# Optimization experiments

Measured on AMD Instinct MI355X. Metric: run time of the kernel, lower is better.

## Reference

```python
import jax, jax.numpy as jnp
import numpy as np

N, H, W = 128, 400, 400          # instances, feature canvas
MS = 28                          # mask_size = pooler_resolution*2
CT, CS = 80, 53                  # thing / stuff classes
STRIDE = 4                       # common_stride
HG, WG = 1600, 1600              # image-resolution gt panoptic
IGNORE = 255
LOSS_W = 1.0


def setup_inputs() -> dict:
    key = jax.random.key(0)
    ks = jax.random.split(key, 8)
    mask_logits = jax.random.normal(ks[0], (N, CT, MS, MS), jnp.float32)
    stuff_logit = jax.random.normal(ks[1], (CS, H, W), jnp.float32)
    thing_logit = jax.random.normal(ks[2], (CT, H, W), jnp.float32)
    # valid boxes in image pixel coords (x0,y0,x2,y2), width/height >= 16 px
    x0 = jax.random.uniform(ks[3], (N,), minval=0.0, maxval=1200.0)
    y0 = jax.random.uniform(ks[4], (N,), minval=0.0, maxval=1200.0)
    wh = jax.random.uniform(ks[5], (N, 2), minval=16.0, maxval=400.0)
    x2 = jnp.minimum(x0 + wh[:, 0], WG - 1.0)
    y2 = jnp.minimum(y0 + wh[:, 1], HG - 1.0)
    bbox = jnp.stack([x0, y0, x2, y2], axis=1).astype(jnp.float32)
    cls_idx = jax.random.randint(ks[6], (N,), 0, CT, dtype=jnp.int32)
    gt_panoptic = jax.random.randint(ks[7], (HG, WG), 0, CS + N, dtype=jnp.int32)
    return {"mask_logits": mask_logits, "stuff_logit": stuff_logit,
            "thing_logit": thing_logit, "bbox": bbox, "cls_idx": cls_idx,
            "gt_panoptic": gt_panoptic}


def _axis_sample(lo, size, grid, src_size):
    """Bilinear sampling coords along one axis (align_corners=False).
    lo: [N] box start (feat px, int); size: [N] box extent; grid: [G].
    Returns (idx0, idx1, frac) each [N, G]."""
    dst = grid[None, :].astype(jnp.float32) - lo[:, None].astype(jnp.float32)
    src = (dst + 0.5) * (src_size / size[:, None].astype(jnp.float32)) - 0.5
    f = jnp.floor(src)
    t = src - f
    i0 = jnp.clip(f, 0, src_size - 1).astype(jnp.int32)
    i1 = jnp.clip(f + 1, 0, src_size - 1).astype(jnp.int32)
    return i0, i1, t


def reference(mask_logits, stuff_logit, thing_logit, bbox, cls_idx, gt_panoptic):
    # _separate_fetch_logits: gather per-instance class channel -> [N, MS, MS]
    ml = mask_logits[jnp.arange(N), cls_idx]

    # _unmap_mask_logit_single: boxes -> feat coords (.long() == floor, boxes >= 0)
    bl = jnp.floor(bbox / STRIDE).astype(jnp.int32)
    x0b, y0b, x2b, y2b = bl[:, 0], bl[:, 1], bl[:, 2], bl[:, 3]
    hh = y2b - y0b + 1
    ww = x2b - x0b + 1
    ys = jnp.arange(H, dtype=jnp.int32)
    xs = jnp.arange(W, dtype=jnp.int32)

    i0, i1, ty = _axis_sample(y0b, hh, ys, MS)   # [N, H]
    j0, j1, tx = _axis_sample(x0b, ww, xs, MS)   # [N, W]

    # separable bilinear: rows [N, H, MS] then cols [N, H, W]
    r0 = jnp.take_along_axis(ml, jnp.broadcast_to(i0[:, :, None], (N, H, MS)), axis=1)
    r1 = jnp.take_along_axis(ml, jnp.broadcast_to(i1[:, :, None], (N, H, MS)), axis=1)
    rows = r0 * (1.0 - ty)[:, :, None] + r1 * ty[:, :, None]
    c0 = jnp.take_along_axis(rows, jnp.broadcast_to(j0[:, None, :], (N, H, W)), axis=2)
    c1 = jnp.take_along_axis(rows, jnp.broadcast_to(j1[:, None, :], (N, H, W)), axis=2)
    val = c0 * (1.0 - tx)[:, None, :] + c1 * tx[:, None, :]

    vy = (ys[None, :] >= jnp.maximum(y0b, 0)[:, None]) & (ys[None, :] <= jnp.minimum(y2b, H - 1)[:, None])
    vx = (xs[None, :] >= jnp.maximum(x0b, 0)[:, None]) & (xs[None, :] <= jnp.minimum(x2b, W - 1)[:, None])
    thing_mask_logit = jnp.where(vy[:, :, None] & vx[:, None, :], val, 0.0)

    # _crop_thing_logit_single: int()/round() based crop window
    bf = bbox / STRIDE
    cx1 = bf[:, 0].astype(jnp.int32)
    cy1 = bf[:, 1].astype(jnp.int32)
    cx2 = (jnp.round(bf[:, 2]) + 1.0).astype(jnp.int32)
    cy2 = (jnp.round(bf[:, 3]) + 1.0).astype(jnp.int32)
    my = (ys[None, :] >= cy1[:, None]) & (ys[None, :] < cy2[:, None])
    mx = (xs[None, :] >= cx1[:, None]) & (xs[None, :] < cx2[:, None])
    thing_sem_logit = jnp.where(my[:, :, None] & mx[:, None, :], thing_logit[cls_idx], 0.0)

    pan_logit = jnp.concatenate(
        [stuff_logit[None], (thing_mask_logit + thing_sem_logit)[None]], axis=1)

    # gt nearest-downsample to feat_size, then CE with ignore_index
    iy = jnp.floor(jnp.arange(H) * (HG / H)).astype(jnp.int32)
    ix = jnp.floor(jnp.arange(W) * (WG / W)).astype(jnp.int32)
    gt_ds = gt_panoptic[iy[:, None], ix[None, :]][None]          # [1, H, W]
    logp = jax.nn.log_softmax(pan_logit, axis=1)
    tgt = jnp.clip(gt_ds, 0, CS + N - 1)
    nll = -jnp.take_along_axis(logp, tgt[:, None], axis=1)[:, 0]  # [1, H, W]
    valid = gt_ds != IGNORE
    pan_loss = LOSS_W * jnp.sum(jnp.where(valid, nll, 0.0)) / jnp.maximum(
        jnp.sum(valid).astype(jnp.float32), 1.0)
    return pan_logit, pan_loss
```

## Files before the change

kernel.cpp:

```cpp
#include <hip/hip_runtime.h>
#include <hip/hip_bf16.h>
#include <math.h>

#define N_   128
#define H_   400
#define W_   400
#define MS_  28
#define CT_  80
#define CS_  53
#define HW_  (H_*W_)
#define NCH_ (CS_ + N_)
#define WG_  1600
#define IGN_ 255
#define G_   8
#define CPG_ 23

struct NParam {
  int vy_lo, vy_hi, vx_lo, vx_hi;
  int cy1, cy2, cx1, cx2;
  float sy, sx;
  int y0b, x0b;
  int mlbase, thbase;
  int pad0, pad1;
};

__device__ NParam g_par[N_];
__device__ float  g_acc[2];
__device__ float  g_pm[G_*HW_];
__device__ float  g_ps[G_*HW_];

__global__ void prep_kernel(const float* __restrict__ bbox,
                            const int*   __restrict__ cls_idx) {
  int n = threadIdx.x;
  if (n < 2) g_acc[n] = 0.0f;
  if (n >= N_) return;
  float b0 = bbox[4*n+0]*0.25f, b1 = bbox[4*n+1]*0.25f,
        b2 = bbox[4*n+2]*0.25f, b3 = bbox[4*n+3]*0.25f;
  int x0b = (int)floorf(b0), y0b = (int)floorf(b1);
  int x2b = (int)floorf(b2), y2b = (int)floorf(b3);
  int hh = y2b - y0b + 1, ww = x2b - x0b + 1;
  NParam p;
  p.vy_lo = max(y0b, 0); p.vy_hi = min(y2b, H_-1);
  p.vx_lo = max(x0b, 0); p.vx_hi = min(x2b, W_-1);
  p.cy1 = (int)b1; p.cx1 = (int)b0;
  p.cy2 = (int)(rintf(b3) + 1.0f);
  p.cx2 = (int)(rintf(b2) + 1.0f);
  p.sy = 28.0f / (float)hh; p.sx = 28.0f / (float)ww;
  p.y0b = y0b; p.x0b = x0b;
  int cls = cls_idx[n];
  p.mlbase = (n*CT_ + cls)*(MS_*MS_);
  p.thbase = cls*HW_;
  p.pad0 = 0; p.pad1 = 0;
  g_par[n] = p;
}

__device__ __forceinline__ void lse_update(float v, float& m, float& s) {
  float d = v - m;
  float e = __expf(-fabsf(d));
  s = (d > 0.0f) ? fmaf(s, e, 1.0f) : (s + e);
  m = fmaxf(m, v);
}

__global__ __launch_bounds__(256) void main_kernel(
    const float* __restrict__ mask_logits,
    const float* __restrict__ stuff_logit,
    const float* __restrict__ thing_logit,
    float* __restrict__ out)
{
  int pix = blockIdx.x*256 + threadIdx.x;
  int y = pix / W_;
  int x = pix - y*W_;
  int grp = blockIdx.y;
  int c0 = grp*CPG_;
  int c1 = min(NCH_, c0 + CPG_);

  float m = -INFINITY, s = 0.0f;

  int c = c0;
  for (; c < min(c1, CS_); ++c) {
    float v = stuff_logit[c*HW_ + pix];
    out[c*HW_ + pix] = v;
    lse_update(v, m, s);
  }
  for (; c < c1; ++c) {
    int n = c - CS_;
    NParam p = g_par[n];
    float v = 0.0f;
    if (y >= p.cy1 && y < p.cy2 && x >= p.cx1 && x < p.cx2)
      v = thing_logit[p.thbase + pix];
    if (y >= p.vy_lo && y <= p.vy_hi && x >= p.vx_lo && x <= p.vx_hi) {
      float srcy = ((float)(y - p.y0b) + 0.5f)*p.sy - 0.5f;
      float fy = floorf(srcy); float ty = srcy - fy;
      int i0 = (int)fminf(fmaxf(fy,        0.0f), (float)(MS_-1));
      int i1 = (int)fminf(fmaxf(fy + 1.0f, 0.0f), (float)(MS_-1));
      float srcx = ((float)(x - p.x0b) + 0.5f)*p.sx - 0.5f;
      float fx = floorf(srcx); float tx = srcx - fx;
      int j0 = (int)fminf(fmaxf(fx,        0.0f), (float)(MS_-1));
      int j1 = (int)fminf(fmaxf(fx + 1.0f, 0.0f), (float)(MS_-1));
      const float* mlp = mask_logits + p.mlbase;
      float a00 = mlp[i0*MS_ + j0], a01 = mlp[i0*MS_ + j1];
      float a10 = mlp[i1*MS_ + j0], a11 = mlp[i1*MS_ + j1];
      float r0 = a00*(1.0f - tx) + a01*tx;
      float r1 = a10*(1.0f - tx) + a11*tx;
      v += r0*(1.0f - ty) + r1*ty;
    }
    out[c*HW_ + pix] = v;
    lse_update(v, m, s);
  }

  g_pm[grp*HW_ + pix] = m;
  g_ps[grp*HW_ + pix] = s;
}

__global__ __launch_bounds__(256) void reduce_kernel(
    const int* __restrict__ gt,
    const float* __restrict__ out_ro,
    float* __restrict__ dummy)
{
  int pix = blockIdx.x*256 + threadIdx.x;

  float m = g_pm[pix], s = g_ps[pix];
  #pragma unroll
  for (int g = 1; g < G_; ++g) {
    float mg = g_pm[g*HW_ + pix];
    float sg = g_ps[g*HW_ + pix];
    float M = fmaxf(m, mg);
    s = s*__expf(m - M) + sg*__expf(mg - M);
    m = M;
  }

  int y = pix / W_;
  int x = pix - y*W_;
  int g = gt[y*(4*WG_) + x*4];
  bool valid = (g != IGN_);
  int tc = min(max(g, 0), NCH_-1);
  float vt = out_ro[tc*HW_ + pix];

  float nll = valid ? (m + __logf(s) - vt) : 0.0f;
  float cnt = valid ? 1.0f : 0.0f;
  for (int off = 32; off >= 1; off >>= 1) {
    nll += __shfl_down(nll, off, 64);
    cnt += __shfl_down(cnt, off, 64);
  }
  __shared__ float red[8];
  int lane = threadIdx.x & 63, wid = threadIdx.x >> 6;
  if (lane == 0) { red[wid*2] = nll; red[wid*2+1] = cnt; }
  __syncthreads();
  if (threadIdx.x == 0) {
    float ts  = red[0] + red[2] + red[4] + red[6];
    float tcn = red[1] + red[3] + red[5] + red[7];
    atomicAdd(&g_acc[0], ts);
    atomicAdd(&g_acc[1], tcn);
  }
  (void)dummy;
}

__global__ void loss_kernel(float* __restrict__ out) {
  if (threadIdx.x == 0) {
    float loss = g_acc[0] / fmaxf(g_acc[1], 1.0f);
    out[NCH_*HW_] = loss;
  }
}

extern "C" void kernel_launch(void* const* d_in, const int* in_sizes, int n_in,
                              void* d_out, int out_size, void* d_ws, size_t ws_size,
                              hipStream_t stream) {
  const float* mask_logits = (const float*)d_in[0];
  const float* stuff_logit = (const float*)d_in[1];
  const float* thing_logit = (const float*)d_in[2];
  const float* bbox        = (const float*)d_in[3];
  const int*   cls_idx     = (const int*)d_in[4];
  const int*   gt          = (const int*)d_in[5];
  float* out = (float*)d_out;

  prep_kernel<<<1, 128, 0, stream>>>(bbox, cls_idx);
  dim3 grid1(HW_/256, G_);
  main_kernel<<<grid1, 256, 0, stream>>>(mask_logits, stuff_logit, thing_logit,
                                         out);
  reduce_kernel<<<HW_/256, 256, 0, stream>>>(gt, out, out);
  loss_kernel<<<1, 64, 0, stream>>>(out);
}
```

Measured before the change: 242.2 us.

## Vectorize to four pixels per thread and fold prep/loss kernels into main/reduce

Each thread now handles four consecutive pixels with float4 loads and stores for stuff, thing and output channels. Per-instance box parameters are computed into shared memory inside every main block instead of in a separate prep kernel. The final loss division moves into the last reduce block through a ticket counter. Together these cut kernel launches and memory transactions, at the cost of redundant per-block parameter setup and relying on the accumulator reset in block (0,0) happening before any reduce atomics.

```diff
diff --git a/kernel.cpp b/kernel.cpp
--- a/kernel.cpp
+++ b/kernel.cpp
@@ -1,5 +1,4 @@
 #include <hip/hip_runtime.h>
-#include <hip/hip_bf16.h>
 #include <math.h>
 
 #define N_   128
@@ -14,6 +13,10 @@
 #define IGN_ 255
 #define G_   8
 #define CPG_ 23
+#define PPT_ 4
+#define BT_  256
+#define PPB_ (BT_*PPT_)
+#define GX_  ((HW_ + PPB_ - 1)/PPB_)
 
 struct NParam {
   int vy_lo, vy_hi, vx_lo, vx_hi;
@@ -24,35 +27,10 @@
   int pad0, pad1;
 };
 
-__device__ NParam g_par[N_];
-__device__ float  g_acc[2];
-__device__ float  g_pm[G_*HW_];
-__device__ float  g_ps[G_*HW_];
-
-__global__ void prep_kernel(const float* __restrict__ bbox,
-                            const int*   __restrict__ cls_idx) {
-  int n = threadIdx.x;
-  if (n < 2) g_acc[n] = 0.0f;
-  if (n >= N_) return;
-  float b0 = bbox[4*n+0]*0.25f, b1 = bbox[4*n+1]*0.25f,
-        b2 = bbox[4*n+2]*0.25f, b3 = bbox[4*n+3]*0.25f;
-  int x0b = (int)floorf(b0), y0b = (int)floorf(b1);
-  int x2b = (int)floorf(b2), y2b = (int)floorf(b3);
-  int hh = y2b - y0b + 1, ww = x2b - x0b + 1;
-  NParam p;
-  p.vy_lo = max(y0b, 0); p.vy_hi = min(y2b, H_-1);
-  p.vx_lo = max(x0b, 0); p.vx_hi = min(x2b, W_-1);
-  p.cy1 = (int)b1; p.cx1 = (int)b0;
-  p.cy2 = (int)(rintf(b3) + 1.0f);
-  p.cx2 = (int)(rintf(b2) + 1.0f);
-  p.sy = 28.0f / (float)hh; p.sx = 28.0f / (float)ww;
-  p.y0b = y0b; p.x0b = x0b;
-  int cls = cls_idx[n];
-  p.mlbase = (n*CT_ + cls)*(MS_*MS_);
-  p.thbase = cls*HW_;
-  p.pad0 = 0; p.pad1 = 0;
-  g_par[n] = p;
-}
+__device__ float        g_acc[2];
+__device__ unsigned int g_done;
+__device__ float        g_pm[G_*HW_];
+__device__ float        g_ps[G_*HW_];
 
 __device__ __forceinline__ void lse_update(float v, float& m, float& s) {
   float d = v - m;
@@ -65,100 +43,164 @@
     const float* __restrict__ mask_logits,
     const float* __restrict__ stuff_logit,
     const float* __restrict__ thing_logit,
+    const float* __restrict__ bbox,
+    const int*   __restrict__ cls_idx,
     float* __restrict__ out)
 {
-  int pix = blockIdx.x*256 + threadIdx.x;
-  int y = pix / W_;
-  int x = pix - y*W_;
+  __shared__ NParam spar[N_];
+  int tid = threadIdx.x;
+  if (blockIdx.x == 0 && blockIdx.y == 0 && tid == 0) {
+    g_acc[0] = 0.0f; g_acc[1] = 0.0f; g_done = 0u;
+  }
+  if (tid < N_) {
+    int n = tid;
+    float b0 = bbox[4*n+0]*0.25f, b1 = bbox[4*n+1]*0.25f,
+          b2 = bbox[4*n+2]*0.25f, b3 = bbox[4*n+3]*0.25f;
+    int x0b = (int)floorf(b0), y0b = (int)floorf(b1);
+    int x2b = (int)floorf(b2), y2b = (int)floorf(b3);
+    int hh = y2b - y0b + 1, ww = x2b - x0b + 1;
+    NParam p;
+    p.vy_lo = max(y0b, 0); p.vy_hi = min(y2b, H_-1);
+    p.vx_lo = max(x0b, 0); p.vx_hi = min(x2b, W_-1);
+    p.cy1 = (int)b1; p.cx1 = (int)b0;
+    p.cy2 = (int)(rintf(b3) + 1.0f);
+    p.cx2 = (int)(rintf(b2) + 1.0f);
+    p.sy = 28.0f / (float)hh; p.sx = 28.0f / (float)ww;
+    p.y0b = y0b; p.x0b = x0b;
+    int cls = cls_idx[n];
+    p.mlbase = (n*CT_ + cls)*(MS_*MS_);
+    p.thbase = cls*HW_;
+    p.pad0 = 0; p.pad1 = 0;
+    spar[n] = p;
+  }
+  __syncthreads();
+
+  int pix0 = (blockIdx.x*BT_ + tid)*PPT_;
+  if (pix0 >= HW_) return;
+  int y  = pix0 / W_;
+  int xb = pix0 - y*W_;
+
   int grp = blockIdx.y;
   int c0 = grp*CPG_;
   int c1 = min(NCH_, c0 + CPG_);
 
-  float m = -INFINITY, s = 0.0f;
+  float mv[PPT_], sv[PPT_];
+  #pragma unroll
+  for (int k = 0; k < PPT_; ++k) { mv[k] = -INFINITY; sv[k] = 0.0f; }
 
   int c = c0;
   for (; c < min(c1, CS_); ++c) {
-    float v = stuff_logit[c*HW_ + pix];
-    out[c*HW_ + pix] = v;
-    lse_update(v, m, s);
+    float4 v = *(const float4*)(stuff_logit + c*HW_ + pix0);
+    *(float4*)(out + c*HW_ + pix0) = v;
+    lse_update(v.x, mv[0], sv[0]);
+    lse_update(v.y, mv[1], sv[1]);
+    lse_update(v.z, mv[2], sv[2]);
+    lse_update(v.w, mv[3], sv[3]);
   }
   for (; c < c1; ++c) {
     int n = c - CS_;
-    NParam p = g_par[n];
-    float v = 0.0f;
-    if (y >= p.cy1 && y < p.cy2 && x >= p.cx1 && x < p.cx2)
-      v = thing_logit[p.thbase + pix];
-    if (y >= p.vy_lo && y <= p.vy_hi && x >= p.vx_lo && x <= p.vx_hi) {
+    NParam p = spar[n];
+    float vv[PPT_] = {0.0f, 0.0f, 0.0f, 0.0f};
+    if (y >= p.cy1 && y < p.cy2 && xb < p.cx2 && xb+PPT_-1 >= p.cx1) {
+      float4 t = *(const float4*)(thing_logit + p.thbase + pix0);
+      float tk[4] = {t.x, t.y, t.z, t.w};
+      #pragma unroll
+      for (int k = 0; k < PPT_; ++k) {
+        int x = xb + k;
+        if (x >= p.cx1 && x < p.cx2) vv[k] = tk[k];
+      }
+    }
+    if (y >= p.vy_lo && y <= p.vy_hi && xb <= p.vx_hi && xb+PPT_-1 >= p.vx_lo) {
       float srcy = ((float)(y - p.y0b) + 0.5f)*p.sy - 0.5f;
       float fy = floorf(srcy); float ty = srcy - fy;
       int i0 = (int)fminf(fmaxf(fy,        0.0f), (float)(MS_-1));
       int i1 = (int)fminf(fmaxf(fy + 1.0f, 0.0f), (float)(MS_-1));
-      float srcx = ((float)(x - p.x0b) + 0.5f)*p.sx - 0.5f;
-      float fx = floorf(srcx); float tx = srcx - fx;
-      int j0 = (int)fminf(fmaxf(fx,        0.0f), (float)(MS_-1));
-      int j1 = (int)fminf(fmaxf(fx + 1.0f, 0.0f), (float)(MS_-1));
-      const float* mlp = mask_logits + p.mlbase;
-      float a00 = mlp[i0*MS_ + j0], a01 = mlp[i0*MS_ + j1];
-      float a10 = mlp[i1*MS_ + j0], a11 = mlp[i1*MS_ + j1];
-      float r0 = a00*(1.0f - tx) + a01*tx;
-      float r1 = a10*(1.0f - tx) + a11*tx;
-      v += r0*(1.0f - ty) + r1*ty;
-    }
-    out[c*HW_ + pix] = v;
-    lse_update(v, m, s);
-  }
-
-  g_pm[grp*HW_ + pix] = m;
-  g_ps[grp*HW_ + pix] = s;
+      const float* r0p = mask_logits + p.mlbase + i0*MS_;
+      const float* r1p = mask_logits + p.mlbase + i1*MS_;
+      #pragma unroll
+      for (int k = 0; k < PPT_; ++k) {
+        int x = xb + k;
+        if (x >= p.vx_lo && x <= p.vx_hi) {
+          float srcx = ((float)(x - p.x0b) + 0.5f)*p.sx - 0.5f;
+          float fx = floorf(srcx); float tx = srcx - fx;
+          int j0 = (int)fminf(fmaxf(fx,        0.0f), (float)(MS_-1));
+          int j1 = (int)fminf(fmaxf(fx + 1.0f, 0.0f), (float)(MS_-1));
+          float r0 = r0p[j0]*(1.0f - tx) + r0p[j1]*tx;
+          float r1 = r1p[j0]*(1.0f - tx) + r1p[j1]*tx;
+          vv[k] += r0*(1.0f - ty) + r1*ty;
+        }
+      }
+    }
+    *(float4*)(out + c*HW_ + pix0) = make_float4(vv[0], vv[1], vv[2], vv[3]);
+    lse_update(vv[0], mv[0], sv[0]);
+    lse_update(vv[1], mv[1], sv[1]);
+    lse_update(vv[2], mv[2], sv[2]);
+    lse_update(vv[3], mv[3], sv[3]);
+  }
+
+  *(float4*)(g_pm + grp*HW_ + pix0) = make_float4(mv[0], mv[1], mv[2], mv[3]);
+  *(float4*)(g_ps + grp*HW_ + pix0) = make_float4(sv[0], sv[1], sv[2], sv[3]);
 }
 
 __global__ __launch_bounds__(256) void reduce_kernel(
     const int* __restrict__ gt,
     const float* __restrict__ out_ro,
-    float* __restrict__ dummy)
+    float* __restrict__ out)
 {
-  int pix = blockIdx.x*256 + threadIdx.x;
-
-  float m = g_pm[pix], s = g_ps[pix];
-  #pragma unroll
-  for (int g = 1; g < G_; ++g) {
-    float mg = g_pm[g*HW_ + pix];
-    float sg = g_ps[g*HW_ + pix];
-    float M = fmaxf(m, mg);
-    s = s*__expf(m - M) + sg*__expf(mg - M);
-    m = M;
-  }
-
-  int y = pix / W_;
-  int x = pix - y*W_;
-  int g = gt[y*(4*WG_) + x*4];
-  bool valid = (g != IGN_);
-  int tc = min(max(g, 0), NCH_-1);
-  float vt = out_ro[tc*HW_ + pix];
-
-  float nll = valid ? (m + __logf(s) - vt) : 0.0f;
-  float cnt = valid ? 1.0f : 0.0f;
+  int tid = threadIdx.x;
+  int pix0 = (blockIdx.x*BT_ + tid)*PPT_;
+  float nll = 0.0f, cnt = 0.0f;
+  if (pix0 < HW_) {
+    float4 m4 = *(const float4*)(g_pm + pix0);
+    float4 s4 = *(const float4*)(g_ps + pix0);
+    float mv[PPT_] = {m4.x, m4.y, m4.z, m4.w};
+    float sv[PPT_] = {s4.x, s4.y, s4.z, s4.w};
+    #pragma unroll
+    for (int g = 1; g < G_; ++g) {
+      float4 mg4 = *(const float4*)(g_pm + g*HW_ + pix0);
+      float4 sg4 = *(const float4*)(g_ps + g*HW_ + pix0);
+      float mg[PPT_] = {mg4.x, mg4.y, mg4.z, mg4.w};
+      float sg[PPT_] = {sg4.x, sg4.y, sg4.z, sg4.w};
+      #pragma unroll
+      for (int k = 0; k < PPT_; ++k) {
+        float M = fmaxf(mv[k], mg[k]);
+        sv[k] = sv[k]*__expf(mv[k] - M) + sg[k]*__expf(mg[k] - M);
+        mv[k] = M;
+      }
+    }
+    int y  = pix0 / W_;
+    int xb = pix0 - y*W_;
+    #pragma unroll
+    for (int k = 0; k < PPT_; ++k) {
+      int g = gt[y*(4*WG_) + (xb + k)*4];
+      bool valid = (g != IGN_);
+      int tc = min(max(g, 0), NCH_-1);
+      float vt = out_ro[tc*HW_ + pix0 + k];
+      nll += valid ? (mv[k] + __logf(sv[k]) - vt) : 0.0f;
+      cnt += valid ? 1.0f : 0.0f;
+    }
+  }
+
   for (int off = 32; off >= 1; off >>= 1) {
     nll += __shfl_down(nll, off, 64);
     cnt += __shfl_down(cnt, off, 64);
   }
   __shared__ float red[8];
-  int lane = threadIdx.x & 63, wid = threadIdx.x >> 6;
+  int lane = tid & 63, wid = tid >> 6;
   if (lane == 0) { red[wid*2] = nll; red[wid*2+1] = cnt; }
   __syncthreads();
-  if (threadIdx.x == 0) {
+  if (tid == 0) {
     float ts  = red[0] + red[2] + red[4] + red[6];
     float tcn = red[1] + red[3] + red[5] + red[7];
     atomicAdd(&g_acc[0], ts);
     atomicAdd(&g_acc[1], tcn);
-  }
-  (void)dummy;
-}
-
-__global__ void loss_kernel(float* __restrict__ out) {
-  if (threadIdx.x == 0) {
-    float loss = g_acc[0] / fmaxf(g_acc[1], 1.0f);
-    out[NCH_*HW_] = loss;
+    __threadfence();
+    unsigned int ticket = atomicAdd(&g_done, 1u);
+    if (ticket == gridDim.x - 1) {
+      __threadfence();
+      float loss = g_acc[0] / fmaxf(g_acc[1], 1.0f);
+      out[NCH_*HW_] = loss;
+    }
   }
 }
 
@@ -173,10 +215,8 @@
   const int*   gt          = (const int*)d_in[5];
   float* out = (float*)d_out;
 
-  prep_kernel<<<1, 128, 0, stream>>>(bbox, cls_idx);
-  dim3 grid1(HW_/256, G_);
-  main_kernel<<<grid1, 256, 0, stream>>>(mask_logits, stuff_logit, thing_logit,
-                                         out);
-  reduce_kernel<<<HW_/256, 256, 0, stream>>>(gt, out, out);
-  loss_kernel<<<1, 64, 0, stream>>>(out);
-}
+  dim3 grid1(GX_, G_);
+  main_kernel<<<grid1, BT_, 0, stream>>>(mask_logits, stuff_logit, thing_logit,
+                                         bbox, cls_idx, out);
+  reduce_kernel<<<GX_, BT_, 0, stream>>>(gt, out, out);
+}
```

After: 226.9 us. 6.3% less time.
